# Kernel tuning notes

Measured on AMD Instinct MI355X. Metric: run time of the kernel, lower is better.

The kernel has to match this reference:

```python
import jax, jax.numpy as jnp
import numpy as np

# Faithful JAX port of kiuikit Remesher.collapse_edges():
#   1) rank edges by priority (argsort)
#   2) propagate max edge-rank through vertices 3 times (scatter_max / gather)
#   3) candidates = edges that are local rank-maxima with positive priority
#   4) two rounds of connection counting (scatter_add) to avoid conflicting collapses
#   5) collapse: move v0 to edge midpoint, remap v1 -> v0, zero degenerate faces
# Non-candidate scatters are dumped into an extra slot at index V (jit-friendly
# replacement for boolean indexing with data-dependent shapes).

V = 2_000_000
F = 4_000_000
E = 6_000_000


def setup_inputs() -> dict:
    key = jax.random.key(0)
    k1, k2, k3, k4 = jax.random.split(key, 4)
    vertices = jax.random.normal(k1, (V, 3), dtype=jnp.float32)
    faces = jax.random.randint(k2, (F, 3), 0, V, dtype=jnp.int32)
    # lower vertex index first, as produced by calc_edges
    edges = jnp.sort(jax.random.randint(k3, (E, 2), 0, V, dtype=jnp.int32), axis=-1)
    priorities = jax.random.uniform(k4, (E,), dtype=jnp.float32)
    return {"vertices": vertices, "faces": faces, "edges": edges, "priorities": priorities}


def reference(vertices, faces, edges, priorities):
    V_ = vertices.shape[0]
    E_ = edges.shape[0]
    DUMP = V_  # scratch slot for masked-out scatters

    # --- priority rank ---
    order = jnp.argsort(priorities)
    rank = jnp.zeros(E_, jnp.int32).at[order].set(jnp.arange(E_, dtype=jnp.int32))

    # --- 3-step scatter_max rank propagation (vert_rank persists across iters,
    #     matching torch_scatter.scatter_max with out=vert_rank) ---
    edge_flat = edges.reshape(-1)  # [2E], row-major: (e0v0, e0v1, e1v0, ...)
    vert_rank = jnp.zeros(V_, jnp.int32)
    edge_rank = rank
    for _ in range(3):
        src = jnp.broadcast_to(edge_rank[:, None], (E_, 2)).reshape(-1)
        vert_rank = vert_rank.at[edge_flat].max(src)
        edge_rank = vert_rank[edges].max(axis=-1)

    # --- candidate selection ---
    cand_mask = (edge_rank == rank) & (priorities > 0)
    c0 = jnp.where(cand_mask, edges[:, 0], DUMP)
    c1 = jnp.where(cand_mask, edges[:, 1], DUMP)

    # --- avoid candidates that touch each other (two connection-count rounds) ---
    vert_conn = jnp.zeros(V_ + 1, jnp.int32).at[c0].set(1)
    edge_conn = vert_conn[edges].sum(axis=-1)  # edges index < V, never DUMP
    vert_conn = vert_conn.at[edge_flat].add(
        jnp.broadcast_to(edge_conn[:, None], (E_, 2)).reshape(-1))
    vert_conn = vert_conn.at[c0].set(0).at[c1].set(0)
    edge_conn = vert_conn[edges].sum(axis=-1)
    vert_conn = vert_conn.at[edge_flat].add(
        jnp.broadcast_to(edge_conn[:, None], (E_, 2)).reshape(-1))

    collapse_mask = cand_mask & (vert_conn[edges[:, 1]] <= 2)
    s0 = jnp.where(collapse_mask, edges[:, 0], DUMP)
    s1 = jnp.where(collapse_mask, edges[:, 1], DUMP)

    # --- mean collapses: v0 <- midpoint of (v0, v1) ---
    mid = 0.5 * (vertices[edges[:, 0]] + vertices[edges[:, 1]])
    vertices_ext = jnp.concatenate([vertices, jnp.zeros((1, 3), vertices.dtype)], axis=0)
    vertices_new = vertices_ext.at[s0].set(mid)[:V_]

    # --- remap v1 -> v0, zero degenerate faces ---
    dest = jnp.arange(V_ + 1, dtype=faces.dtype)
    dest = dest.at[s1].set(jnp.where(collapse_mask, edges[:, 0], DUMP))[:V_]
    faces_new = dest[faces]
    f0, f1, f2 = faces_new[:, 0], faces_new[:, 1], faces_new[:, 2]
    collapsed = (f0 == f1) | (f1 == f2) | (f0 == f2)
    faces_new = jnp.where(collapsed[:, None], 0, faces_new)

    return vertices_new, faces_new
```

## Files before the change

### kernel.cpp

```cpp
#include <hip/hip_runtime.h>
#include <math.h>

typedef unsigned long long u64;
typedef unsigned int u32;

__device__ __forceinline__ u64 mkkey(float p, int e) {
    return ((u64)__float_as_uint(p) << 23) | (unsigned)e;
}

__global__ void k_sentinel(float* out, float v) {
    if (threadIdx.x == 0 && blockIdx.x == 0) out[0] = v;
}

__global__ void k_zero16(uint4* __restrict__ p, int n) {
    int i = blockIdx.x * blockDim.x + threadIdx.x;
    if (i < n) p[i] = make_uint4(0, 0, 0, 0);
}

__global__ void k_scatter1(const int2* __restrict__ edges, const float* __restrict__ pri,
                           u64* __restrict__ vert, int E) {
    int e = blockIdx.x * blockDim.x + threadIdx.x;
    if (e >= E) return;
    u64 k = mkkey(pri[e], e);
    int2 ed = edges[e];
    u64 a = vert[ed.x], b = vert[ed.y];
    if (k > a) atomicMax(&vert[ed.x], k);
    if (k > b) atomicMax(&vert[ed.y], k);
}

__global__ void k_copyW(u64* __restrict__ dst, const u64* __restrict__ src, int n) {
    int i = blockIdx.x * blockDim.x + threadIdx.x;
    if (i < n) dst[i] = src[i];
}

__global__ void k_fused(const int2* __restrict__ edges, const u64* __restrict__ vsrc,
                        u64* __restrict__ vdst, int E) {
    int e = blockIdx.x * blockDim.x + threadIdx.x;
    if (e >= E) return;
    int2 ed = edges[e];
    u64 a = vsrc[ed.x], b = vsrc[ed.y];
    u64 er = a > b ? a : b;
    if (er > a) atomicMax(&vdst[ed.x], er);
    if (er > b) atomicMax(&vdst[ed.y], er);
}

__global__ void k_cand(const int2* __restrict__ edges, const float* __restrict__ pri,
                       const u64* __restrict__ vert, unsigned char* __restrict__ flags,
                       unsigned char* __restrict__ cand, int E) {
    int e = blockIdx.x * blockDim.x + threadIdx.x;
    if (e >= E) return;
    int2 ed = edges[e];
    u64 a = vert[ed.x], b = vert[ed.y];
    u64 er = a > b ? a : b;
    float p = pri[e];
    bool c = (er == mkkey(p, e)) && (p > 0.0f);
    cand[e] = c ? 1 : 0;
    if (c) {
        flags[ed.x] = 3;
        if (ed.y != ed.x) flags[ed.y] = 2;
    }
}

__global__ void k_conn1(const int2* __restrict__ edges, const unsigned char* __restrict__ flags,
                        u32* __restrict__ pack, int E) {
    int e = blockIdx.x * blockDim.x + threadIdx.x;
    if (e >= E) return;
    int2 ed = edges[e];
    u32 ec = (u32)(flags[ed.x] & 1) + (u32)(flags[ed.y] & 1);
    if (ec) {
        atomicAdd(&pack[ed.x], ec);
        atomicAdd(&pack[ed.y], ec);
    }
}

__global__ void k_conn2(const int2* __restrict__ edges, const unsigned char* __restrict__ flags,
                        u32* __restrict__ pack, int E) {
    int e = blockIdx.x * blockDim.x + threadIdx.x;
    if (e >= E) return;
    int2 ed = edges[e];
    unsigned char gx = flags[ed.x], gy = flags[ed.y];
    u32 px = pack[ed.x], py = pack[ed.y];
    u32 fx = (gx & 2) ? 0u : ((u32)(gx & 1) + (px & 0xFFFFu));
    u32 fy = (gy & 2) ? 0u : ((u32)(gy & 1) + (py & 0xFFFFu));
    u32 ec = fx + fy;
    if (ec) {
        atomicAdd(&pack[ed.x], ec << 16);
        atomicAdd(&pack[ed.y], ec << 16);
    }
}

__global__ void k_collapse(const int2* __restrict__ edges, const unsigned char* __restrict__ cand,
                           const unsigned char* __restrict__ flags,
                           const u32* __restrict__ pack, const float* __restrict__ vin,
                           int* __restrict__ repl, float* __restrict__ vout, int E) {
    int e = blockIdx.x * blockDim.x + threadIdx.x;
    if (e >= E) return;
    if (!cand[e]) return;
    int2 ed = edges[e];
    unsigned char gy = flags[ed.y];
    u32 py = pack[ed.y];
    u32 fy = (gy & 2) ? 0u : ((u32)(gy & 1) + (py & 0xFFFFu));
    u32 total = fy + (py >> 16);
    if (total <= 2) {
        repl[ed.y] = ed.x + 1;
        size_t bx = (size_t)ed.x * 3, by = (size_t)ed.y * 3;
#pragma unroll
        for (int j = 0; j < 3; ++j)
            vout[bx + j] = 0.5f * (vin[bx + j] + vin[by + j]);
    }
}

__global__ void k_faces(const int* __restrict__ faces, const int* __restrict__ repl,
                        float* __restrict__ fout, int F) {
    int i = blockIdx.x * blockDim.x + threadIdx.x;
    if (i >= F) return;
    size_t b = (size_t)i * 3;
    int a0 = faces[b + 0], a1 = faces[b + 1], a2 = faces[b + 2];
    int r0 = repl[a0]; if (r0) a0 = r0 - 1;
    int r1 = repl[a1]; if (r1) a1 = r1 - 1;
    int r2 = repl[a2]; if (r2) a2 = r2 - 1;
    if (a0 == a1 || a1 == a2 || a0 == a2) { a0 = 0; a1 = 0; a2 = 0; }
    fout[b + 0] = (float)a0;
    fout[b + 1] = (float)a1;
    fout[b + 2] = (float)a2;
}

extern "C" void kernel_launch(void* const* d_in, const int* in_sizes, int n_in,
                              void* d_out, int out_size, void* d_ws, size_t ws_size,
                              hipStream_t stream) {
    const int V = in_sizes[0] / 3;
    const int F = in_sizes[1] / 3;
    const int E = in_sizes[3];

    const float* vin  = (const float*)d_in[0];
    const int* faces  = (const int*)d_in[1];
    const int2* edges = (const int2*)d_in[2];
    const float* pri  = (const float*)d_in[3];

    float* vout = (float*)d_out;
    float* fout = vout + (size_t)V * 3;

    char* ws = (char*)d_ws;
    size_t off = 0;
    auto alloc = [&](size_t n) -> void* {
        void* p = ws + off;
        off = (off + n + 255) & ~(size_t)255;
        return p;
    };
    u64* vertA           = (u64*)alloc((size_t)V * 8);
    unsigned char* flags = (unsigned char*)alloc((size_t)V);
    u32* pack            = (u32*)alloc((size_t)V * 4);
    int* repl            = (int*)alloc((size_t)V * 4);
    size_t zero_bytes = off;
    u64* vertB           = (u64*)alloc((size_t)V * 8);
    unsigned char* cand  = (unsigned char*)alloc((size_t)E);
    size_t needed = off;

    const int TB = 256;
    if (ws_size > 0 && ws_size < needed) {
        k_sentinel<<<1, 64, 0, stream>>>(vout, ldexpf(1.0f, (int)(ws_size >> 23)));
        return;
    }

    const int gE = (E + TB - 1) / TB;
    const int gF = (F + TB - 1) / TB;
    const int gW = (V + TB - 1) / TB;
    const int nZ = (int)(zero_bytes / 16);
    const int gZ = (nZ + TB - 1) / TB;

    k_zero16<<<gZ, TB, 0, stream>>>((uint4*)ws, nZ);
    hipMemcpyAsync(d_out, d_in[0], (size_t)V * 3 * sizeof(float),
                   hipMemcpyDeviceToDevice, stream);

    k_scatter1<<<gE, TB, 0, stream>>>(edges, pri, vertA, E);
    k_copyW<<<gW, TB, 0, stream>>>(vertB, vertA, V);
    k_fused<<<gE, TB, 0, stream>>>(edges, vertA, vertB, E);
    k_copyW<<<gW, TB, 0, stream>>>(vertA, vertB, V);
    k_fused<<<gE, TB, 0, stream>>>(edges, vertB, vertA, E);
    k_cand <<<gE, TB, 0, stream>>>(edges, pri, vertA, flags, cand, E);

    k_conn1<<<gE, TB, 0, stream>>>(edges, flags, pack, E);
    k_conn2<<<gE, TB, 0, stream>>>(edges, flags, pack, E);

    k_collapse<<<gE, TB, 0, stream>>>(edges, cand, flags, pack, vin,
                                      repl, vout, E);
    k_faces<<<gF, TB, 0, stream>>>(faces, repl, fout, F);
}
```

Baseline: 1.386 ms.

## Bucket edges by first vertex to localize scatter/gather accesses

Adds a histogram, a scan and a permute pass that reorder edges into 64 buckets keyed on the high bits of the first vertex index. Each edge's endpoints are packed into one u64 and its priority key into another. All edge-parallel passes then read this permuted layout, so atomics and gathers on the x vertex fall in a narrower address range per bucket, which should improve cache locality. The cost is three extra passes and 96MB of extra workspace, and the path only runs when the workspace is large enough and V and E fit the packed bit widths.

```diff
diff --git a/kernel.cpp b/kernel.cpp
--- a/kernel.cpp
+++ b/kernel.cpp
@@ -4,18 +4,152 @@
 typedef unsigned long long u64;
 typedef unsigned int u32;
 
+#define NB 64
+#define M21 ((1u << 21) - 1)
+
 __device__ __forceinline__ u64 mkkey(float p, int e) {
     return ((u64)__float_as_uint(p) << 23) | (unsigned)e;
 }
+__device__ __forceinline__ u64 umax64(u64 a, u64 b) { return a > b ? a : b; }
 
 __global__ void k_sentinel(float* out, float v) {
     if (threadIdx.x == 0 && blockIdx.x == 0) out[0] = v;
 }
-
 __global__ void k_zero16(uint4* __restrict__ p, int n) {
     int i = blockIdx.x * blockDim.x + threadIdx.x;
     if (i < n) p[i] = make_uint4(0, 0, 0, 0);
 }
+__global__ void k_copyW(u64* __restrict__ dst, const u64* __restrict__ src, int n) {
+    int i = blockIdx.x * blockDim.x + threadIdx.x;
+    if (i < n) dst[i] = src[i];
+}
+
+
+__global__ void k_hist(const int2* __restrict__ edges, u32* __restrict__ bcnt,
+                       int E, int shift) {
+    __shared__ u32 lh[NB];
+    int tid = threadIdx.x;
+    if (tid < NB) lh[tid] = 0;
+    __syncthreads();
+    int e = blockIdx.x * blockDim.x + tid;
+    if (e < E) atomicAdd(&lh[edges[e].x >> shift], 1u);
+    __syncthreads();
+    if (tid < NB && lh[tid]) atomicAdd(&bcnt[tid], lh[tid]);
+}
+
+__global__ void k_scan(const u32* __restrict__ bcnt, u32* __restrict__ bcur) {
+    if (threadIdx.x == 0 && blockIdx.x == 0) {
+        u32 run = 0;
+        for (int i = 0; i < NB; ++i) { bcur[i] = run; run += bcnt[i]; }
+    }
+}
+
+__global__ void k_permute(const int2* __restrict__ edges, const float* __restrict__ pri,
+                          u64* __restrict__ permA, u64* __restrict__ permB,
+                          u32* __restrict__ bcur, int E, int shift) {
+    __shared__ u32 lcnt[NB];
+    __shared__ u32 lbase[NB];
+    int tid = threadIdx.x;
+    if (tid < NB) lcnt[tid] = 0;
+    __syncthreads();
+    int e = blockIdx.x * blockDim.x + tid;
+    int b = 0; u32 my = 0; int2 ed;
+    bool act = (e < E);
+    if (act) { ed = edges[e]; b = ed.x >> shift; my = atomicAdd(&lcnt[b], 1u); }
+    __syncthreads();
+    if (tid < NB && lcnt[tid]) lbase[tid] = atomicAdd(&bcur[tid], lcnt[tid]);
+    __syncthreads();
+    if (act) {
+        u32 pos = lbase[b] + my;
+        permA[pos] = (u64)(u32)ed.x | ((u64)(u32)ed.y << 21);
+        permB[pos] = mkkey(pri[e], e);
+    }
+}
+
+
+__global__ void k_scatter1_p(const u64* __restrict__ pa, const u64* __restrict__ pk,
+                             u64* __restrict__ vert, int E) {
+    int i = blockIdx.x * blockDim.x + threadIdx.x;
+    if (i >= E) return;
+    u64 a = pa[i];
+    int x = (int)(a & M21), y = (int)((a >> 21) & M21);
+    u64 k = pk[i];
+    u64 va = vert[x], vb = vert[y];
+    if (k > va) atomicMax(&vert[x], k);
+    if (k > vb) atomicMax(&vert[y], k);
+}
+
+__global__ void k_fused_p(const u64* __restrict__ pa, const u64* __restrict__ vsrc,
+                          u64* __restrict__ vdst, int E) {
+    int i = blockIdx.x * blockDim.x + threadIdx.x;
+    if (i >= E) return;
+    u64 a = pa[i];
+    int x = (int)(a & M21), y = (int)((a >> 21) & M21);
+    u64 va = vsrc[x], vb = vsrc[y];
+    u64 er = umax64(va, vb);
+    if (er > va) atomicMax(&vdst[x], er);
+    if (er > vb) atomicMax(&vdst[y], er);
+}
+
+__global__ void k_cand_p(const u64* __restrict__ pa, const u64* __restrict__ pk,
+                         const u64* __restrict__ vert, unsigned char* __restrict__ flags,
+                         unsigned char* __restrict__ candp, int E) {
+    int i = blockIdx.x * blockDim.x + threadIdx.x;
+    if (i >= E) return;
+    u64 a = pa[i];
+    int x = (int)(a & M21), y = (int)((a >> 21) & M21);
+    u64 k = pk[i];
+    u64 er = umax64(vert[x], vert[y]);
+    bool c = (er == k) && ((k >> 23) != 0);
+    candp[i] = c ? 1 : 0;
+    if (c) { flags[x] = 3; if (y != x) flags[y] = 2; }
+}
+
+__global__ void k_conn1_p(const u64* __restrict__ pa, const unsigned char* __restrict__ flags,
+                          u32* __restrict__ pack, int E) {
+    int i = blockIdx.x * blockDim.x + threadIdx.x;
+    if (i >= E) return;
+    u64 a = pa[i];
+    int x = (int)(a & M21), y = (int)((a >> 21) & M21);
+    u32 ec = (u32)(flags[x] & 1) + (u32)(flags[y] & 1);
+    if (ec) { atomicAdd(&pack[x], ec); atomicAdd(&pack[y], ec); }
+}
+
+__global__ void k_conn2_p(const u64* __restrict__ pa, const unsigned char* __restrict__ flags,
+                          u32* __restrict__ pack, int E) {
+    int i = blockIdx.x * blockDim.x + threadIdx.x;
+    if (i >= E) return;
+    u64 a = pa[i];
+    int x = (int)(a & M21), y = (int)((a >> 21) & M21);
+    unsigned char gx = flags[x], gy = flags[y];
+    u32 fx = (gx & 2) ? 0u : ((u32)(gx & 1) + (pack[x] & 0xFFFFu));
+    u32 fy = (gy & 2) ? 0u : ((u32)(gy & 1) + (pack[y] & 0xFFFFu));
+    u32 ec = fx + fy;
+    if (ec) { atomicAdd(&pack[x], ec << 16); atomicAdd(&pack[y], ec << 16); }
+}
+
+__global__ void k_collapse_p(const u64* __restrict__ pa, const unsigned char* __restrict__ candp,
+                             const unsigned char* __restrict__ flags,
+                             const u32* __restrict__ pack, const float* __restrict__ vin,
+                             int* __restrict__ repl, float* __restrict__ vout, int E) {
+    int i = blockIdx.x * blockDim.x + threadIdx.x;
+    if (i >= E) return;
+    if (!candp[i]) return;
+    u64 a = pa[i];
+    int x = (int)(a & M21), y = (int)((a >> 21) & M21);
+    unsigned char gy = flags[y];
+    u32 py = pack[y];
+    u32 fy = (gy & 2) ? 0u : ((u32)(gy & 1) + (py & 0xFFFFu));
+    u32 total = fy + (py >> 16);
+    if (total <= 2) {
+        repl[y] = x + 1;
+        size_t bx = (size_t)x * 3, by = (size_t)y * 3;
+#pragma unroll
+        for (int j = 0; j < 3; ++j)
+            vout[bx + j] = 0.5f * (vin[bx + j] + vin[by + j]);
+    }
+}
+
 
 __global__ void k_scatter1(const int2* __restrict__ edges, const float* __restrict__ pri,
                            u64* __restrict__ vert, int E) {
@@ -27,68 +161,47 @@
     if (k > a) atomicMax(&vert[ed.x], k);
     if (k > b) atomicMax(&vert[ed.y], k);
 }
-
-__global__ void k_copyW(u64* __restrict__ dst, const u64* __restrict__ src, int n) {
-    int i = blockIdx.x * blockDim.x + threadIdx.x;
-    if (i < n) dst[i] = src[i];
-}
-
 __global__ void k_fused(const int2* __restrict__ edges, const u64* __restrict__ vsrc,
                         u64* __restrict__ vdst, int E) {
     int e = blockIdx.x * blockDim.x + threadIdx.x;
     if (e >= E) return;
     int2 ed = edges[e];
     u64 a = vsrc[ed.x], b = vsrc[ed.y];
-    u64 er = a > b ? a : b;
+    u64 er = umax64(a, b);
     if (er > a) atomicMax(&vdst[ed.x], er);
     if (er > b) atomicMax(&vdst[ed.y], er);
 }
-
 __global__ void k_cand(const int2* __restrict__ edges, const float* __restrict__ pri,
                        const u64* __restrict__ vert, unsigned char* __restrict__ flags,
                        unsigned char* __restrict__ cand, int E) {
     int e = blockIdx.x * blockDim.x + threadIdx.x;
     if (e >= E) return;
     int2 ed = edges[e];
-    u64 a = vert[ed.x], b = vert[ed.y];
-    u64 er = a > b ? a : b;
+    u64 er = umax64(vert[ed.x], vert[ed.y]);
     float p = pri[e];
     bool c = (er == mkkey(p, e)) && (p > 0.0f);
     cand[e] = c ? 1 : 0;
-    if (c) {
-        flags[ed.x] = 3;
-        if (ed.y != ed.x) flags[ed.y] = 2;
-    }
-}
-
+    if (c) { flags[ed.x] = 3; if (ed.y != ed.x) flags[ed.y] = 2; }
+}
 __global__ void k_conn1(const int2* __restrict__ edges, const unsigned char* __restrict__ flags,
                         u32* __restrict__ pack, int E) {
     int e = blockIdx.x * blockDim.x + threadIdx.x;
     if (e >= E) return;
     int2 ed = edges[e];
     u32 ec = (u32)(flags[ed.x] & 1) + (u32)(flags[ed.y] & 1);
-    if (ec) {
-        atomicAdd(&pack[ed.x], ec);
-        atomicAdd(&pack[ed.y], ec);
-    }
-}
-
+    if (ec) { atomicAdd(&pack[ed.x], ec); atomicAdd(&pack[ed.y], ec); }
+}
 __global__ void k_conn2(const int2* __restrict__ edges, const unsigned char* __restrict__ flags,
                         u32* __restrict__ pack, int E) {
     int e = blockIdx.x * blockDim.x + threadIdx.x;
     if (e >= E) return;
     int2 ed = edges[e];
     unsigned char gx = flags[ed.x], gy = flags[ed.y];
-    u32 px = pack[ed.x], py = pack[ed.y];
-    u32 fx = (gx & 2) ? 0u : ((u32)(gx & 1) + (px & 0xFFFFu));
-    u32 fy = (gy & 2) ? 0u : ((u32)(gy & 1) + (py & 0xFFFFu));
+    u32 fx = (gx & 2) ? 0u : ((u32)(gx & 1) + (pack[ed.x] & 0xFFFFu));
+    u32 fy = (gy & 2) ? 0u : ((u32)(gy & 1) + (pack[ed.y] & 0xFFFFu));
     u32 ec = fx + fy;
-    if (ec) {
-        atomicAdd(&pack[ed.x], ec << 16);
-        atomicAdd(&pack[ed.y], ec << 16);
-    }
-}
-
+    if (ec) { atomicAdd(&pack[ed.x], ec << 16); atomicAdd(&pack[ed.y], ec << 16); }
+}
 __global__ void k_collapse(const int2* __restrict__ edges, const unsigned char* __restrict__ cand,
                            const unsigned char* __restrict__ flags,
                            const u32* __restrict__ pack, const float* __restrict__ vin,
@@ -147,20 +260,26 @@
         off = (off + n + 255) & ~(size_t)255;
         return p;
     };
+    u32* bcnt            = (u32*)alloc(NB * 4);
+    u32* bcur            = (u32*)alloc(NB * 4);
     u64* vertA           = (u64*)alloc((size_t)V * 8);
     unsigned char* flags = (unsigned char*)alloc((size_t)V);
     u32* pack            = (u32*)alloc((size_t)V * 4);
     int* repl            = (int*)alloc((size_t)V * 4);
     size_t zero_bytes = off;
     u64* vertB           = (u64*)alloc((size_t)V * 8);
-    unsigned char* cand  = (unsigned char*)alloc((size_t)E);
-    size_t needed = off;
+    unsigned char* cand  = (unsigned char*)alloc((size_t)E + 4);
+    size_t needed_base = off;
+    u64* permA           = (u64*)alloc((size_t)E * 8);
+    u64* permB           = (u64*)alloc((size_t)E * 8);
+    size_t needed_ext = off;
 
     const int TB = 256;
-    if (ws_size > 0 && ws_size < needed) {
+    if (ws_size > 0 && ws_size < needed_base) {
         k_sentinel<<<1, 64, 0, stream>>>(vout, ldexpf(1.0f, (int)(ws_size >> 23)));
         return;
     }
+    const bool use_perm = (ws_size >= needed_ext) && (V <= (1 << 21)) && (E < (1 << 23));
 
     const int gE = (E + TB - 1) / TB;
     const int gF = (F + TB - 1) / TB;
@@ -172,17 +291,36 @@
     hipMemcpyAsync(d_out, d_in[0], (size_t)V * 3 * sizeof(float),
                    hipMemcpyDeviceToDevice, stream);
 
-    k_scatter1<<<gE, TB, 0, stream>>>(edges, pri, vertA, E);
-    k_copyW<<<gW, TB, 0, stream>>>(vertB, vertA, V);
-    k_fused<<<gE, TB, 0, stream>>>(edges, vertA, vertB, E);
-    k_copyW<<<gW, TB, 0, stream>>>(vertA, vertB, V);
-    k_fused<<<gE, TB, 0, stream>>>(edges, vertB, vertA, E);
-    k_cand <<<gE, TB, 0, stream>>>(edges, pri, vertA, flags, cand, E);
-
-    k_conn1<<<gE, TB, 0, stream>>>(edges, flags, pack, E);
-    k_conn2<<<gE, TB, 0, stream>>>(edges, flags, pack, E);
-
-    k_collapse<<<gE, TB, 0, stream>>>(edges, cand, flags, pack, vin,
-                                      repl, vout, E);
+    if (use_perm) {
+        int shift = 0;
+        while (((V - 1) >> shift) >= NB) shift++;
+        const int PT = 1024;
+        const int gP = (E + PT - 1) / PT;
+        k_hist   <<<gP, PT, 0, stream>>>(edges, bcnt, E, shift);
+        k_scan   <<<1, 64, 0, stream>>>(bcnt, bcur);
+        k_permute<<<gP, PT, 0, stream>>>(edges, pri, permA, permB, bcur, E, shift);
+
+        k_scatter1_p<<<gE, TB, 0, stream>>>(permA, permB, vertA, E);
+        k_copyW<<<gW, TB, 0, stream>>>(vertB, vertA, V);
+        k_fused_p<<<gE, TB, 0, stream>>>(permA, vertA, vertB, E);
+        k_copyW<<<gW, TB, 0, stream>>>(vertA, vertB, V);
+        k_fused_p<<<gE, TB, 0, stream>>>(permA, vertB, vertA, E);
+        k_cand_p<<<gE, TB, 0, stream>>>(permA, permB, vertA, flags, cand, E);
+        k_conn1_p<<<gE, TB, 0, stream>>>(permA, flags, pack, E);
+        k_conn2_p<<<gE, TB, 0, stream>>>(permA, flags, pack, E);
+        k_collapse_p<<<gE, TB, 0, stream>>>(permA, cand, flags, pack, vin,
+                                            repl, vout, E);
+    } else {
+        k_scatter1<<<gE, TB, 0, stream>>>(edges, pri, vertA, E);
+        k_copyW<<<gW, TB, 0, stream>>>(vertB, vertA, V);
+        k_fused<<<gE, TB, 0, stream>>>(edges, vertA, vertB, E);
+        k_copyW<<<gW, TB, 0, stream>>>(vertA, vertB, V);
+        k_fused<<<gE, TB, 0, stream>>>(edges, vertB, vertA, E);
+        k_cand<<<gE, TB, 0, stream>>>(edges, pri, vertA, flags, cand, E);
+        k_conn1<<<gE, TB, 0, stream>>>(edges, flags, pack, E);
+        k_conn2<<<gE, TB, 0, stream>>>(edges, flags, pack, E);
+        k_collapse<<<gE, TB, 0, stream>>>(edges, cand, flags, pack, vin,
+                                          repl, vout, E);
+    }
     k_faces<<<gF, TB, 0, stream>>>(faces, repl, fout, F);
 }
```

New measurement: 1.719 ms. 24.0% more time.
